# Kernel optimization log

Measured on AMD Instinct MI355X. Metric: run time of the kernel, lower is better.

The kernel has to match this reference:

```python
import jax, jax.numpy as jnp
import numpy as np

# Graph geometry: G complete graphs (molecules) of n nodes each.
N_PER_G, G, DEG = 64, 256, 16
H, D = 8, 8
IN_DIM = H * D      # 64
EDGE_DIM = 64
N = N_PER_G * G                      # 16384 nodes
EF = G * N_PER_G * N_PER_G           # 1,048,576 full edges
ES = G * N_PER_G * DEG               # 262,144 sparse edges
SCALE = float(np.sqrt(D))


def _edges():
    n = N_PER_G
    # full graph: all (i -> j) pairs per block, edge id = b*n*n + i*n + j
    ij = np.arange(n * n)
    i, j = ij // n, ij % n
    b = np.arange(G)[:, None]
    src_full = (b * n + i[None, :]).reshape(-1).astype(np.int32)
    dst_full = (b * n + j[None, :]).reshape(-1).astype(np.int32)
    # sparse graph: each dst j receives from DEG distinct sources (j+1..j+DEG mod n)
    jj = np.arange(n)[:, None]
    kk = np.arange(DEG)[None, :]
    ii = (jj + 1 + kk) % n
    eid_block = (ii * n + jj).reshape(-1)                 # [n*DEG]
    sparse_eid = (np.arange(G)[:, None] * n * n + eid_block[None, :]).reshape(-1).astype(np.int32)
    return jnp.asarray(src_full), jnp.asarray(dst_full), jnp.asarray(sparse_eid)


def setup_inputs() -> dict:
    key = jax.random.key(0)
    ks = jax.random.split(key, 16)
    w = lambda k, shape, s=0.05: s * jax.random.normal(k, shape, jnp.float32)
    src_full, dst_full, sparse_eid = _edges()
    return dict(
        h=jax.random.normal(ks[0], (N, IN_DIM), jnp.float32),
        e=jax.random.normal(ks[1], (ES, EDGE_DIM), jnp.float32),
        adj2=jax.random.uniform(ks[2], (EF,), jnp.float32),
        rel_pos_3d=jax.random.normal(ks[3], (EF, H), jnp.float32),
        Wq=w(ks[4], (H * D, IN_DIM)), bq=jnp.zeros((H * D,), jnp.float32),
        Wk=w(ks[5], (H * D, IN_DIM)), bk=jnp.zeros((H * D,), jnp.float32),
        Wv=w(ks[6], (H * D, IN_DIM)), bv=jnp.zeros((H * D,), jnp.float32),
        Wpe=w(ks[7], (H, EDGE_DIM)), bpe=jnp.zeros((H,), jnp.float32),
        Wap=w(ks[8], (EDGE_DIM, H)), bap=jnp.zeros((EDGE_DIM,), jnp.float32),
        Wo=w(ks[9], (H * D, H * D)), bo=jnp.zeros((H * D,), jnp.float32),
        Woe=w(ks[10], (EDGE_DIM, EDGE_DIM)), boe=jnp.zeros((EDGE_DIM,), jnp.float32),
        src_full=src_full, dst_full=dst_full, sparse_eid=sparse_eid,
    )


def reference(h, e, adj2, rel_pos_3d, Wq, bq, Wk, bk, Wv, bv, Wpe, bpe,
              Wap, bap, Wo, bo, Woe, boe, src_full, dst_full, sparse_eid):
    Qh = (h @ Wq.T + bq).reshape(N, H, D)
    Kh = (h @ Wk.T + bk).reshape(N, H, D)
    Vh = (h @ Wv.T + bv).reshape(N, H, D)
    proj_e = e @ Wpe.T + bpe                                   # [ES, H]
    # edge-wise QK dot (src=K, dst=Q), scaled, then gaussian-decay + rel-pos bias
    score = jnp.sum(Kh[src_full] * Qh[dst_full], axis=-1) / SCALE   # [EF, H]
    score = score * adj2[:, None] + rel_pos_3d                      # [EF, H]
    # gather sparse-subgraph scores, project for edge output, add proj_e bias
    sc_sp = score[sparse_eid]                                        # [ES, H]
    e_out_raw = sc_sp @ Wap.T + bap                                  # [ES, EDGE_DIM]
    score = score.at[sparse_eid].set(sc_sp + proj_e)
    # edge softmax over incoming edges of each destination node
    logits = jnp.clip(score, -5.0, 5.0)
    m = jax.ops.segment_max(logits, dst_full, num_segments=N)
    ex = jnp.exp(logits - m[dst_full])
    den = jax.ops.segment_sum(ex, dst_full, num_segments=N)
    attn = ex / den[dst_full]                                        # [EF, H]
    # weighted scatter-sum of source values
    wV = jax.ops.segment_sum(Vh[src_full] * attn[..., None], dst_full, num_segments=N)
    h_out = wV.reshape(N, H * D) @ Wo.T + bo
    e_out = (e_out_raw + e) @ Woe.T + boe
    return h_out, e_out
```

## Files before the change

kernel.cpp:

```cpp
#include <hip/hip_runtime.h>


__global__ __launch_bounds__(512, 2) void qkvpe_kernel(
    const float* __restrict__ h,
    const float* __restrict__ e,
    const float* __restrict__ Wq, const float* __restrict__ bq,
    const float* __restrict__ Wk, const float* __restrict__ bk,
    const float* __restrict__ Wv, const float* __restrict__ bv,
    const float* __restrict__ Wpe, const float* __restrict__ bpe,
    float* __restrict__ Qs, float* __restrict__ Ks, float* __restrict__ Vs,
    float* __restrict__ PEs)
{
    const int t = threadIdx.x;
    if (blockIdx.x < 256) {
        const int b    = blockIdx.x;
        const int lane = t & 63;
        const int wu   = __builtin_amdgcn_readfirstlane(t >> 6);
        const float* hrow = h + (size_t)(b * 64 + lane) * 64;
        float accQ[8], accK[8], accV[8];
        #pragma unroll
        for (int cc = 0; cc < 8; ++cc) {
            const int c = wu * 8 + cc;
            accQ[cc] = bq[c]; accK[cc] = bk[c]; accV[cc] = bv[c];
        }
        #pragma unroll 1
        for (int k0 = 0; k0 < 4; ++k0) {
            float hv[16];
            #pragma unroll
            for (int u = 0; u < 4; ++u) {
                const float4 x = ((const float4*)hrow)[k0 * 4 + u];
                hv[u*4+0] = x.x; hv[u*4+1] = x.y; hv[u*4+2] = x.z; hv[u*4+3] = x.w;
            }
            #pragma unroll
            for (int cc = 0; cc < 8; ++cc) {
                const int c = wu * 8 + cc;
                const float* wq  = Wq + c * 64 + k0 * 16;
                const float* wk  = Wk + c * 64 + k0 * 16;
                const float* wvp = Wv + c * 64 + k0 * 16;
                #pragma unroll
                for (int k = 0; k < 16; ++k) {
                    accQ[cc] = fmaf(hv[k], wq[k],  accQ[cc]);
                    accK[cc] = fmaf(hv[k], wk[k],  accK[cc]);
                    accV[cc] = fmaf(hv[k], wvp[k], accV[cc]);
                }
            }
        }
        const size_t o = (size_t)(b * 64 + lane) * 64 + wu * 8;
        *(float4*)(Qs + o)     = make_float4(accQ[0], accQ[1], accQ[2], accQ[3]);
        *(float4*)(Qs + o + 4) = make_float4(accQ[4], accQ[5], accQ[6], accQ[7]);
        *(float4*)(Ks + o)     = make_float4(accK[0], accK[1], accK[2], accK[3]);
        *(float4*)(Ks + o + 4) = make_float4(accK[4], accK[5], accK[6], accK[7]);
        *(float4*)(Vs + o)     = make_float4(accV[0], accV[1], accV[2], accV[3]);
        *(float4*)(Vs + o + 4) = make_float4(accV[4], accV[5], accV[6], accV[7]);
    } else {
        const int row = (blockIdx.x - 256) * 512 + t;
        const float* erow = e + (size_t)row * 64;
        float acc[8];
        #pragma unroll
        for (int h2 = 0; h2 < 8; ++h2) acc[h2] = bpe[h2];
        #pragma unroll 1
        for (int k0 = 0; k0 < 4; ++k0) {
            float ev[16];
            #pragma unroll
            for (int u = 0; u < 4; ++u) {
                const float4 x = ((const float4*)erow)[k0 * 4 + u];
                ev[u*4+0] = x.x; ev[u*4+1] = x.y; ev[u*4+2] = x.z; ev[u*4+3] = x.w;
            }
            #pragma unroll
            for (int h2 = 0; h2 < 8; ++h2) {
                const float* wp = Wpe + h2 * 64 + k0 * 16;
                #pragma unroll
                for (int k = 0; k < 16; ++k)
                    acc[h2] = fmaf(ev[k], wp[k], acc[h2]);
            }
        }
        float* p0 = PEs + (size_t)row * 8;
        *(float4*)(p0)     = make_float4(acc[0], acc[1], acc[2], acc[3]);
        *(float4*)(p0 + 4) = make_float4(acc[4], acc[5], acc[6], acc[7]);
    }
}

__global__ __launch_bounds__(1024, 2) void attn_kernel(
    const float* __restrict__ Qs, const float* __restrict__ Ks,
    const float* __restrict__ Vs, const float* __restrict__ PEs,
    const float* __restrict__ adj2,
    const float* __restrict__ rel,
    const float* __restrict__ Wo, const float* __restrict__ bo,
    float* __restrict__ h_out,
    float* __restrict__ scsp)
{
    __shared__ float shK[64 * 64];
    __shared__ float shV[64 * 64];
    __shared__ float shPE[512 * 8];
    __shared__ float shRed[256 * 9];

    const int b2   = blockIdx.x;
    const int b    = b2 >> 1;
    const int joff = (b2 & 1) << 5;
    const int t    = threadIdx.x;

    const int j_local = (t >> 3) & 31;
    const int hh      = t & 7;
    const int q4      = t >> 8;
    const int j       = joff + j_local;

    {
        const int r  = t >> 4;
        const int gh = t & 15;
        const int g  = gh >> 1, lo = (gh & 1) * 4;
        const int d  = r * 64 + ((g ^ (r & 7)) << 3) + lo;
        const int so = r * 64 + g * 8 + lo;
        shK[d + 0] = Ks[(size_t)b * 4096 + so + 0];
        shK[d + 1] = Ks[(size_t)b * 4096 + so + 1];
        shK[d + 2] = Ks[(size_t)b * 4096 + so + 2];
        shK[d + 3] = Ks[(size_t)b * 4096 + so + 3];
        shV[d + 0] = Vs[(size_t)b * 4096 + so + 0];
        shV[d + 1] = Vs[(size_t)b * 4096 + so + 1];
        shV[d + 2] = Vs[(size_t)b * 4096 + so + 2];
        shV[d + 3] = Vs[(size_t)b * 4096 + so + 3];
        *(float4*)&shPE[t * 4] =
            *(const float4*)(PEs + ((size_t)b * 1024 + joff * 16) * 8 + t * 4);
    }
    float q[8];
    {
        const float* qp = Qs + (size_t)(b * 64 + j) * 64 + hh * 8;
        const float4 a = *(const float4*)qp;
        const float4 c = *(const float4*)(qp + 4);
        q[0]=a.x; q[1]=a.y; q[2]=a.z; q[3]=a.w;
        q[4]=c.x; q[5]=c.y; q[6]=c.z; q[7]=c.w;
    }
    __syncthreads();

    float den = 0.f;
    float wv[8] = {0.f,0.f,0.f,0.f,0.f,0.f,0.f,0.f};
    const float* relP = rel  + (size_t)b * 32768 + (size_t)(joff + j_local) * 8 + hh;
    const float* adjP = adj2 + (size_t)b * 4096 + j;
    const float inv_scale = 0.35355339059327379f;
    #pragma unroll 4
    for (int it = 0; it < 16; ++it) {
        const int i  = (q4 << 4) + it;
        const float rp = relP[(size_t)i * 512];
        const float a2 = adjP[(size_t)i * 64];
        const int kb = i * 64 + ((hh ^ (i & 7)) << 3);
        const float4 kA = *(const float4*)&shK[kb];
        const float4 kB = *(const float4*)&shK[kb + 4];
        float s;
        s = kA.x * q[0];
        s = fmaf(kA.y, q[1], s); s = fmaf(kA.z, q[2], s); s = fmaf(kA.w, q[3], s);
        s = fmaf(kB.x, q[4], s); s = fmaf(kB.y, q[5], s); s = fmaf(kB.z, q[6], s);
        s = fmaf(kB.w, q[7], s);
        s = fmaf(s * inv_scale, a2, rp);
        const int kidx = (i - j - 1) & 63;
        if (kidx < 16) {
            const int x = (j_local * 16 + kidx) * 8 + hh;
            const float pe = shPE[x];
            shPE[x] = s;
            s += pe;
        }
        s = fminf(fmaxf(s, -5.f), 5.f);
        const float ex = __expf(s);
        den += ex;
        const float4 vA = *(const float4*)&shV[kb];
        const float4 vB = *(const float4*)&shV[kb + 4];
        wv[0] = fmaf(ex, vA.x, wv[0]); wv[1] = fmaf(ex, vA.y, wv[1]);
        wv[2] = fmaf(ex, vA.z, wv[2]); wv[3] = fmaf(ex, vA.w, wv[3]);
        wv[4] = fmaf(ex, vB.x, wv[4]); wv[5] = fmaf(ex, vB.y, wv[5]);
        wv[6] = fmaf(ex, vB.z, wv[6]); wv[7] = fmaf(ex, vB.w, wv[7]);
    }
    const int jh = t & 255;
    if (q4 == 0) {
        #pragma unroll
        for (int u = 0; u < 8; ++u) shRed[jh * 9 + u] = wv[u];
        shRed[jh * 9 + 8] = den;
    }
    __syncthreads();
    if (q4 == 1) {
        #pragma unroll
        for (int u = 0; u < 8; ++u) shRed[jh * 9 + u] += wv[u];
        shRed[jh * 9 + 8] += den;
    }
    __syncthreads();
    if (q4 == 2) {
        #pragma unroll
        for (int u = 0; u < 8; ++u) shRed[jh * 9 + u] += wv[u];
        shRed[jh * 9 + 8] += den;
    }
    __syncthreads();
    if (q4 == 3) {
        #pragma unroll
        for (int u = 0; u < 8; ++u) shRed[jh * 9 + u] += wv[u];
        shRed[jh * 9 + 8] += den;
    }
    __syncthreads();

    {
        const int row = t >> 1, pp = t & 1;
        *(float4*)(scsp + (size_t)((size_t)b * 1024 + joff * 16 + row) * 8 + pp * 4) =
            *(const float4*)&shPE[row * 8 + pp * 4];
    }
    if (t < 256) {
        const float* rd = &shRed[t * 9];
        const float id = 1.f / rd[8];
        float* wp = &shK[(t >> 3) * 64 + (t & 7) * 8];
        *(float4*)(wp)     = make_float4(rd[0]*id, rd[1]*id, rd[2]*id, rd[3]*id);
        *(float4*)(wp + 4) = make_float4(rd[4]*id, rd[5]*id, rd[6]*id, rd[7]*id);
    }
    __syncthreads();

    {
        const int rl = t >> 5;
        const int c0 = (t & 31) * 2;
        float acc[2];
        acc[0] = bo[c0]; acc[1] = bo[c0 + 1];
        #pragma unroll 1
        for (int k0 = 0; k0 < 4; ++k0) {
            float tv[16];
            #pragma unroll
            for (int u = 0; u < 4; ++u) {
                const float4 x = *(const float4*)&shK[rl * 64 + k0 * 16 + u * 4];
                tv[u*4+0] = x.x; tv[u*4+1] = x.y; tv[u*4+2] = x.z; tv[u*4+3] = x.w;
            }
            #pragma unroll
            for (int u = 0; u < 2; ++u) {
                const float* wo = Wo + (c0 + u) * 64 + k0 * 16;
                #pragma unroll
                for (int k = 0; k < 16; ++k)
                    acc[u] = fmaf(tv[k], wo[k], acc[u]);
            }
        }
        float* orow = h_out + (size_t)(b * 64 + joff + rl) * 64 + c0;
        *(float2*)orow = make_float2(acc[0], acc[1]);
    }
}

__global__ void prep_kernel(const float* __restrict__ Wap, const float* __restrict__ bap,
                            const float* __restrict__ Woe, const float* __restrict__ boe,
                            float* __restrict__ M2, float* __restrict__ Tm, int hasT)
{
    const int tg = blockIdx.x * 64 + threadIdx.x;
    if (tg < 512) {
        const int c = tg >> 3, hq = tg & 7;
        float s = 0.f;
        #pragma unroll 8
        for (int k = 0; k < 64; ++k) s = fmaf(Woe[c * 64 + k], Wap[k * 8 + hq], s);
        M2[tg] = s;
    } else if (tg < 576) {
        const int c = tg - 512;
        float s = boe[c];
        #pragma unroll 8
        for (int k = 0; k < 64; ++k) s = fmaf(bap[k], Woe[c * 64 + k], s);
        M2[512 + c] = s;
    } else if (hasT && tg < 576 + 73 * 64) {
        const int idx = tg - 576;
        const int k = idx >> 6, c = idx & 63;
        float v;
        if (k < 64) {
            v = Woe[c * 64 + k];
        } else if (k < 72) {
            const int hq = k - 64;
            v = 0.f;
            #pragma unroll 8
            for (int kk = 0; kk < 64; ++kk)
                v = fmaf(Woe[c * 64 + kk], Wap[kk * 8 + hq], v);
        } else {
            v = boe[c];
            #pragma unroll 8
            for (int kk = 0; kk < 64; ++kk)
                v = fmaf(bap[kk], Woe[c * 64 + kk], v);
        }
        Tm[k * 64 + c] = v;
    }
}

__global__ __launch_bounds__(256, 2) void eoutT_kernel(
    const float* __restrict__ e,
    const float* __restrict__ scsp,
    const float* __restrict__ Tm,
    float* __restrict__ e_out)
{
    __shared__ float shET[72 * 69];
    __shared__ float shTm[73 * 64];

    const int t    = threadIdx.x;
    const int base = blockIdx.x * 64;

    {
        const int r0 = t >> 2, qq = t & 3;
        const float* ep = e + (size_t)(base + r0) * 64 + qq * 16;
        #pragma unroll
        for (int v = 0; v < 4; ++v) {
            const float4 x = ((const float4*)ep)[v];
            const int c = qq * 16 + v * 4;
            shET[(c + 0) * 69 + r0] = x.x;
            shET[(c + 1) * 69 + r0] = x.y;
            shET[(c + 2) * 69 + r0] = x.z;
            shET[(c + 3) * 69 + r0] = x.w;
        }
    }
    if (t < 128) {
        const int r = t >> 1, pp = t & 1;
        const float4 s4 = *(const float4*)(scsp + (size_t)(base + r) * 8 + pp * 4);
        shET[(64 + pp * 4 + 0) * 69 + r] = s4.x;
        shET[(64 + pp * 4 + 1) * 69 + r] = s4.y;
        shET[(64 + pp * 4 + 2) * 69 + r] = s4.z;
        shET[(64 + pp * 4 + 3) * 69 + r] = s4.w;
    }
    #pragma unroll
    for (int v = 0; v < 5; ++v) {
        const int fi = v * 256 + t;
        if (fi < 1168)
            *(float4*)&shTm[fi * 4] = *(const float4*)(Tm + fi * 4);
    }
    __syncthreads();

    const int rq = t >> 4;
    const int cq = t & 15;

    float acc[16];
    {
        const float4 bcv = *(const float4*)&shTm[72 * 64 + cq * 4];
        #pragma unroll
        for (int ri = 0; ri < 4; ++ri) {
            acc[ri*4+0] = bcv.x; acc[ri*4+1] = bcv.y;
            acc[ri*4+2] = bcv.z; acc[ri*4+3] = bcv.w;
        }
    }
    #pragma unroll
    for (int k = 0; k < 72; ++k) {
        const float4 ev = *(const float4*)&shET[k * 69 + rq * 4];
        const float4 wk = *(const float4*)&shTm[k * 64 + cq * 4];
        acc[0]  = fmaf(ev.x, wk.x, acc[0]);  acc[1]  = fmaf(ev.x, wk.y, acc[1]);
        acc[2]  = fmaf(ev.x, wk.z, acc[2]);  acc[3]  = fmaf(ev.x, wk.w, acc[3]);
        acc[4]  = fmaf(ev.y, wk.x, acc[4]);  acc[5]  = fmaf(ev.y, wk.y, acc[5]);
        acc[6]  = fmaf(ev.y, wk.z, acc[6]);  acc[7]  = fmaf(ev.y, wk.w, acc[7]);
        acc[8]  = fmaf(ev.z, wk.x, acc[8]);  acc[9]  = fmaf(ev.z, wk.y, acc[9]);
        acc[10] = fmaf(ev.z, wk.z, acc[10]); acc[11] = fmaf(ev.z, wk.w, acc[11]);
        acc[12] = fmaf(ev.w, wk.x, acc[12]); acc[13] = fmaf(ev.w, wk.y, acc[13]);
        acc[14] = fmaf(ev.w, wk.z, acc[14]); acc[15] = fmaf(ev.w, wk.w, acc[15]);
    }
    #pragma unroll
    for (int ri = 0; ri < 4; ++ri) {
        float* orow = e_out + (size_t)(base + rq * 4 + ri) * 64 + cq * 4;
        *(float4*)orow = make_float4(acc[ri*4+0], acc[ri*4+1], acc[ri*4+2], acc[ri*4+3]);
    }
}

__global__ __launch_bounds__(256, 2) void eout_kernel(
    const float* __restrict__ e,
    const float* __restrict__ scsp,
    const float* __restrict__ Woe,
    const float* __restrict__ M2g,
    float* __restrict__ e_out)
{
    __shared__ float shE[64 * 64];
    __shared__ float shS[64 * 8];
    const int t    = threadIdx.x;
    const int base = blockIdx.x * 64;
    {
        const int r = t >> 2, qq = t & 3;
        const float* ep = e + (size_t)(base + r) * 64 + qq * 16;
        #pragma unroll
        for (int u = 0; u < 4; ++u) {
            const float4 x = ((const float4*)ep)[u];
            const int cc = qq * 4 + u;
            *(float4*)&shE[r * 64 + ((cc ^ (r & 15)) << 2)] = x;
        }
    }
    if (t < 128) {
        const int r = t >> 1, pp = t & 1;
        *(float4*)&shS[r * 8 + pp * 4] =
            *(const float4*)(scsp + (size_t)(base + r) * 8 + pp * 4);
    }
    __syncthreads();
    const int w = __builtin_amdgcn_readfirstlane(t >> 6);
    const int r = t & 63;
    float sc[8];
    {
        const float4 a  = *(const float4*)&shS[r * 8];
        const float4 c4 = *(const float4*)&shS[r * 8 + 4];
        sc[0]=a.x; sc[1]=a.y; sc[2]=a.z; sc[3]=a.w;
        sc[4]=c4.x; sc[5]=c4.y; sc[6]=c4.z; sc[7]=c4.w;
    }
    float acc[16];
    #pragma unroll
    for (int u = 0; u < 16; ++u) {
        const int c = w * 16 + u;
        float s = M2g[512 + c];
        #pragma unroll
        for (int hq = 0; hq < 8; ++hq)
            s = fmaf(sc[hq], M2g[c * 8 + hq], s);
        acc[u] = s;
    }
    #pragma unroll
    for (int k0 = 0; k0 < 4; ++k0) {
        float ev[16];
        #pragma unroll
        for (int v = 0; v < 4; ++v) {
            const int cc = k0 * 4 + v;
            const float4 x = *(const float4*)&shE[r * 64 + ((cc ^ (r & 15)) << 2)];
            ev[v*4+0] = x.x; ev[v*4+1] = x.y; ev[v*4+2] = x.z; ev[v*4+3] = x.w;
        }
        #pragma unroll
        for (int u = 0; u < 16; ++u) {
            const float* wr = Woe + (w * 16 + u) * 64 + k0 * 16;
            #pragma unroll
            for (int k = 0; k < 16; ++k)
                acc[u] = fmaf(ev[k], wr[k], acc[u]);
        }
    }
    float* orow = e_out + (size_t)(base + r) * 64 + w * 16;
    #pragma unroll
    for (int u = 0; u < 4; ++u)
        *(float4*)&orow[u * 4] =
            make_float4(acc[u*4+0], acc[u*4+1], acc[u*4+2], acc[u*4+3]);
}

extern "C" void kernel_launch(void* const* d_in, const int* in_sizes, int n_in,
                              void* d_out, int out_size, void* d_ws, size_t ws_size,
                              hipStream_t stream) {
    const float* h    = (const float*)d_in[0];
    const float* e    = (const float*)d_in[1];
    const float* adj2 = (const float*)d_in[2];
    const float* rel  = (const float*)d_in[3];
    const float* Wq   = (const float*)d_in[4];  const float* bq  = (const float*)d_in[5];
    const float* Wk   = (const float*)d_in[6];  const float* bk  = (const float*)d_in[7];
    const float* Wv   = (const float*)d_in[8];  const float* bv  = (const float*)d_in[9];
    const float* Wpe  = (const float*)d_in[10]; const float* bpe = (const float*)d_in[11];
    const float* Wap  = (const float*)d_in[12]; const float* bap = (const float*)d_in[13];
    const float* Wo   = (const float*)d_in[14]; const float* bo  = (const float*)d_in[15];
    const float* Woe  = (const float*)d_in[16]; const float* boe = (const float*)d_in[17];

    float* out  = (float*)d_out;
    float* hout = out;
    float* eout = out + 16384 * 64;
    float* Qs   = eout;
    float* Ks   = eout + 1048576;
    float* Vs   = eout + 2097152;
    float* PEs  = eout + 3145728;
    float* ws   = (float*)d_ws;
    float* scsp = ws;
    float* M2g  = ws + 2097152;
    float* Tm   = ws + 2098176;
    const int hasT = (ws_size >= (size_t)(2098176 + 73 * 64) * sizeof(float)) ? 1 : 0;

    prep_kernel<<<dim3(82), dim3(64), 0, stream>>>(Wap, bap, Woe, boe, M2g, Tm, hasT);
    qkvpe_kernel<<<dim3(768), dim3(512), 0, stream>>>(
        h, e, Wq, bq, Wk, bk, Wv, bv, Wpe, bpe, Qs, Ks, Vs, PEs);
    attn_kernel<<<dim3(512), dim3(1024), 0, stream>>>(
        Qs, Ks, Vs, PEs, adj2, rel, Wo, bo, hout, scsp);
    if (hasT)
        eoutT_kernel<<<dim3(4096), dim3(256), 0, stream>>>(e, scsp, Tm, eout);
    else
        eout_kernel<<<dim3(4096), dim3(256), 0, stream>>>(e, scsp, Woe, M2g, eout);
}
```

Before: 130.9 us.

## Restructure attention so each thread loops all sources; split output projection into own kernel

The attention kernel now assigns one thread per (destination, head) pair and loops over all 64 sources. The loop starts at the 16 sparse neighbours so the edge-bias add and score capture happen in registers. This removes the LDS staging of K/V/PE, the four-way shared-memory reduction and its barriers. K and V are read straight from global/cache, and the normalized wV is written to the h_out buffer. A new hout_kernel then applies Wo in place with a register-tiled shared-memory GEMM. The trade-offs are a quarter as many threads, longer serial loops, and rel/adj accesses that now vary the source index per lane and so coalesce less well. It also adds an extra launch and a global round trip for wV.

```diff
diff --git a/kernel.cpp b/kernel.cpp
--- a/kernel.cpp
+++ b/kernel.cpp
@@ -80,47 +80,27 @@
     }
 }
 
-__global__ __launch_bounds__(1024, 2) void attn_kernel(
+__global__ __launch_bounds__(256, 2) void attn_kernel(
     const float* __restrict__ Qs, const float* __restrict__ Ks,
     const float* __restrict__ Vs, const float* __restrict__ PEs,
     const float* __restrict__ adj2,
     const float* __restrict__ rel,
-    const float* __restrict__ Wo, const float* __restrict__ bo,
-    float* __restrict__ h_out,
+    float* __restrict__ wVg,
     float* __restrict__ scsp)
 {
-    __shared__ float shK[64 * 64];
-    __shared__ float shV[64 * 64];
-    __shared__ float shPE[512 * 8];
-    __shared__ float shRed[256 * 9];
-
     const int b2   = blockIdx.x;
     const int b    = b2 >> 1;
     const int joff = (b2 & 1) << 5;
     const int t    = threadIdx.x;
-
-    const int j_local = (t >> 3) & 31;
-    const int hh      = t & 7;
-    const int q4      = t >> 8;
-    const int j       = joff + j_local;
-
-    {
-        const int r  = t >> 4;
-        const int gh = t & 15;
-        const int g  = gh >> 1, lo = (gh & 1) * 4;
-        const int d  = r * 64 + ((g ^ (r & 7)) << 3) + lo;
-        const int so = r * 64 + g * 8 + lo;
-        shK[d + 0] = Ks[(size_t)b * 4096 + so + 0];
-        shK[d + 1] = Ks[(size_t)b * 4096 + so + 1];
-        shK[d + 2] = Ks[(size_t)b * 4096 + so + 2];
-        shK[d + 3] = Ks[(size_t)b * 4096 + so + 3];
-        shV[d + 0] = Vs[(size_t)b * 4096 + so + 0];
-        shV[d + 1] = Vs[(size_t)b * 4096 + so + 1];
-        shV[d + 2] = Vs[(size_t)b * 4096 + so + 2];
-        shV[d + 3] = Vs[(size_t)b * 4096 + so + 3];
-        *(float4*)&shPE[t * 4] =
-            *(const float4*)(PEs + ((size_t)b * 1024 + joff * 16) * 8 + t * 4);
-    }
+    const int j    = joff + (t >> 3);
+    const int hh   = t & 7;
+
+    const float* kB   = Ks + (size_t)b * 4096 + hh * 8;
+    const float* vB   = Vs + (size_t)b * 4096 + hh * 8;
+    const float* relP = rel + ((size_t)b * 4096 + j) * 8 + hh;
+    const float* adjP = adj2 + (size_t)b * 4096 + j;
+    const float* peP  = PEs + ((size_t)b * 1024 + j * 16) * 8 + hh;
+
     float q[8];
     {
         const float* qp = Qs + (size_t)(b * 64 + j) * 64 + hh * 8;
@@ -129,107 +109,137 @@
         q[0]=a.x; q[1]=a.y; q[2]=a.z; q[3]=a.w;
         q[4]=c.x; q[5]=c.y; q[6]=c.z; q[7]=c.w;
     }
-    __syncthreads();
 
     float den = 0.f;
     float wv[8] = {0.f,0.f,0.f,0.f,0.f,0.f,0.f,0.f};
-    const float* relP = rel  + (size_t)b * 32768 + (size_t)(joff + j_local) * 8 + hh;
-    const float* adjP = adj2 + (size_t)b * 4096 + j;
+    float sc[16];
     const float inv_scale = 0.35355339059327379f;
-    #pragma unroll 4
-    for (int it = 0; it < 16; ++it) {
-        const int i  = (q4 << 4) + it;
+
+    #pragma unroll
+    for (int m = 0; m < 16; ++m) {
+        const int i = (j + 1 + m) & 63;
+        const float4 kA = *(const float4*)(kB + i * 64);
+        const float4 kBv = *(const float4*)(kB + i * 64 + 4);
         const float rp = relP[(size_t)i * 512];
         const float a2 = adjP[(size_t)i * 64];
-        const int kb = i * 64 + ((hh ^ (i & 7)) << 3);
-        const float4 kA = *(const float4*)&shK[kb];
-        const float4 kB = *(const float4*)&shK[kb + 4];
-        float s;
-        s = kA.x * q[0];
+        const float pe = peP[m * 8];
+        float s = kA.x * q[0];
         s = fmaf(kA.y, q[1], s); s = fmaf(kA.z, q[2], s); s = fmaf(kA.w, q[3], s);
-        s = fmaf(kB.x, q[4], s); s = fmaf(kB.y, q[5], s); s = fmaf(kB.z, q[6], s);
-        s = fmaf(kB.w, q[7], s);
+        s = fmaf(kBv.x, q[4], s); s = fmaf(kBv.y, q[5], s); s = fmaf(kBv.z, q[6], s);
+        s = fmaf(kBv.w, q[7], s);
         s = fmaf(s * inv_scale, a2, rp);
-        const int kidx = (i - j - 1) & 63;
-        if (kidx < 16) {
-            const int x = (j_local * 16 + kidx) * 8 + hh;
-            const float pe = shPE[x];
-            shPE[x] = s;
-            s += pe;
-        }
+        sc[m] = s;
+        s += pe;
         s = fminf(fmaxf(s, -5.f), 5.f);
         const float ex = __expf(s);
         den += ex;
-        const float4 vA = *(const float4*)&shV[kb];
-        const float4 vB = *(const float4*)&shV[kb + 4];
+        const float4 vA = *(const float4*)(vB + i * 64);
+        const float4 vBv = *(const float4*)(vB + i * 64 + 4);
         wv[0] = fmaf(ex, vA.x, wv[0]); wv[1] = fmaf(ex, vA.y, wv[1]);
         wv[2] = fmaf(ex, vA.z, wv[2]); wv[3] = fmaf(ex, vA.w, wv[3]);
-        wv[4] = fmaf(ex, vB.x, wv[4]); wv[5] = fmaf(ex, vB.y, wv[5]);
-        wv[6] = fmaf(ex, vB.z, wv[6]); wv[7] = fmaf(ex, vB.w, wv[7]);
-    }
-    const int jh = t & 255;
-    if (q4 == 0) {
-        #pragma unroll
-        for (int u = 0; u < 8; ++u) shRed[jh * 9 + u] = wv[u];
-        shRed[jh * 9 + 8] = den;
+        wv[4] = fmaf(ex, vBv.x, wv[4]); wv[5] = fmaf(ex, vBv.y, wv[5]);
+        wv[6] = fmaf(ex, vBv.z, wv[6]); wv[7] = fmaf(ex, vBv.w, wv[7]);
+    }
+    #pragma unroll 8
+    for (int m = 16; m < 64; ++m) {
+        const int i = (j + 1 + m) & 63;
+        const float4 kA = *(const float4*)(kB + i * 64);
+        const float4 kBv = *(const float4*)(kB + i * 64 + 4);
+        const float rp = relP[(size_t)i * 512];
+        const float a2 = adjP[(size_t)i * 64];
+        float s = kA.x * q[0];
+        s = fmaf(kA.y, q[1], s); s = fmaf(kA.z, q[2], s); s = fmaf(kA.w, q[3], s);
+        s = fmaf(kBv.x, q[4], s); s = fmaf(kBv.y, q[5], s); s = fmaf(kBv.z, q[6], s);
+        s = fmaf(kBv.w, q[7], s);
+        s = fmaf(s * inv_scale, a2, rp);
+        s = fminf(fmaxf(s, -5.f), 5.f);
+        const float ex = __expf(s);
+        den += ex;
+        const float4 vA = *(const float4*)(vB + i * 64);
+        const float4 vBv = *(const float4*)(vB + i * 64 + 4);
+        wv[0] = fmaf(ex, vA.x, wv[0]); wv[1] = fmaf(ex, vA.y, wv[1]);
+        wv[2] = fmaf(ex, vA.z, wv[2]); wv[3] = fmaf(ex, vA.w, wv[3]);
+        wv[4] = fmaf(ex, vBv.x, wv[4]); wv[5] = fmaf(ex, vBv.y, wv[5]);
+        wv[6] = fmaf(ex, vBv.z, wv[6]); wv[7] = fmaf(ex, vBv.w, wv[7]);
+    }
+
+    float* sp = scsp + ((size_t)b * 1024 + j * 16) * 8 + hh;
+    #pragma unroll
+    for (int m = 0; m < 16; ++m) sp[m * 8] = sc[m];
+
+    const float id = 1.f / den;
+    float* wp = wVg + (size_t)(b * 64 + j) * 64 + hh * 8;
+    *(float4*)(wp)     = make_float4(wv[0]*id, wv[1]*id, wv[2]*id, wv[3]*id);
+    *(float4*)(wp + 4) = make_float4(wv[4]*id, wv[5]*id, wv[6]*id, wv[7]*id);
+}
+
+__global__ __launch_bounds__(256, 2) void hout_kernel(
+    const float* __restrict__ wVg,
+    const float* __restrict__ Wo, const float* __restrict__ bo,
+    float* __restrict__ h_out)
+{
+    __shared__ float shWT[64 * 69];
+    __shared__ float shWoT[64 * 65];
+
+    const int t    = threadIdx.x;
+    const int base = blockIdx.x * 64;
+
+    {
+        const int r0 = t >> 2, qq = t & 3;
+        const float* ep = wVg + (size_t)(base + r0) * 64 + qq * 16;
+        #pragma unroll
+        for (int v = 0; v < 4; ++v) {
+            const float4 x = ((const float4*)ep)[v];
+            const int c = qq * 16 + v * 4;
+            shWT[(c + 0) * 69 + r0] = x.x;
+            shWT[(c + 1) * 69 + r0] = x.y;
+            shWT[(c + 2) * 69 + r0] = x.z;
+            shWT[(c + 3) * 69 + r0] = x.w;
+        }
+    }
+    {
+        const int c0 = t >> 2, qq = t & 3;
+        const float* wp = Wo + c0 * 64 + qq * 16;
+        #pragma unroll
+        for (int v = 0; v < 4; ++v) {
+            const float4 x = ((const float4*)wp)[v];
+            const int k = qq * 16 + v * 4;
+            shWoT[(k + 0) * 65 + c0] = x.x;
+            shWoT[(k + 1) * 65 + c0] = x.y;
+            shWoT[(k + 2) * 65 + c0] = x.z;
+            shWoT[(k + 3) * 65 + c0] = x.w;
+        }
     }
     __syncthreads();
-    if (q4 == 1) {
-        #pragma unroll
-        for (int u = 0; u < 8; ++u) shRed[jh * 9 + u] += wv[u];
-        shRed[jh * 9 + 8] += den;
-    }
-    __syncthreads();
-    if (q4 == 2) {
-        #pragma unroll
-        for (int u = 0; u < 8; ++u) shRed[jh * 9 + u] += wv[u];
-        shRed[jh * 9 + 8] += den;
-    }
-    __syncthreads();
-    if (q4 == 3) {
-        #pragma unroll
-        for (int u = 0; u < 8; ++u) shRed[jh * 9 + u] += wv[u];
-        shRed[jh * 9 + 8] += den;
-    }
-    __syncthreads();
-
-    {
-        const int row = t >> 1, pp = t & 1;
-        *(float4*)(scsp + (size_t)((size_t)b * 1024 + joff * 16 + row) * 8 + pp * 4) =
-            *(const float4*)&shPE[row * 8 + pp * 4];
-    }
-    if (t < 256) {
-        const float* rd = &shRed[t * 9];
-        const float id = 1.f / rd[8];
-        float* wp = &shK[(t >> 3) * 64 + (t & 7) * 8];
-        *(float4*)(wp)     = make_float4(rd[0]*id, rd[1]*id, rd[2]*id, rd[3]*id);
-        *(float4*)(wp + 4) = make_float4(rd[4]*id, rd[5]*id, rd[6]*id, rd[7]*id);
-    }
-    __syncthreads();
-
-    {
-        const int rl = t >> 5;
-        const int c0 = (t & 31) * 2;
-        float acc[2];
-        acc[0] = bo[c0]; acc[1] = bo[c0 + 1];
-        #pragma unroll 1
-        for (int k0 = 0; k0 < 4; ++k0) {
-            float tv[16];
-            #pragma unroll
-            for (int u = 0; u < 4; ++u) {
-                const float4 x = *(const float4*)&shK[rl * 64 + k0 * 16 + u * 4];
-                tv[u*4+0] = x.x; tv[u*4+1] = x.y; tv[u*4+2] = x.z; tv[u*4+3] = x.w;
-            }
-            #pragma unroll
-            for (int u = 0; u < 2; ++u) {
-                const float* wo = Wo + (c0 + u) * 64 + k0 * 16;
-                #pragma unroll
-                for (int k = 0; k < 16; ++k)
-                    acc[u] = fmaf(tv[k], wo[k], acc[u]);
-            }
-        }
-        float* orow = h_out + (size_t)(b * 64 + joff + rl) * 64 + c0;
-        *(float2*)orow = make_float2(acc[0], acc[1]);
+
+    const int rq = t >> 4;
+    const int cq = t & 15;
+    float acc[16];
+    {
+        const float4 bv = *(const float4*)(bo + cq * 4);
+        #pragma unroll
+        for (int ri = 0; ri < 4; ++ri) {
+            acc[ri*4+0] = bv.x; acc[ri*4+1] = bv.y;
+            acc[ri*4+2] = bv.z; acc[ri*4+3] = bv.w;
+        }
+    }
+    #pragma unroll
+    for (int k = 0; k < 64; ++k) {
+        const float4 ev = *(const float4*)&shWT[k * 69 + rq * 4];
+        const float4 wk = *(const float4*)&shWoT[k * 65 + cq * 4];
+        acc[0]  = fmaf(ev.x, wk.x, acc[0]);  acc[1]  = fmaf(ev.x, wk.y, acc[1]);
+        acc[2]  = fmaf(ev.x, wk.z, acc[2]);  acc[3]  = fmaf(ev.x, wk.w, acc[3]);
+        acc[4]  = fmaf(ev.y, wk.x, acc[4]);  acc[5]  = fmaf(ev.y, wk.y, acc[5]);
+        acc[6]  = fmaf(ev.y, wk.z, acc[6]);  acc[7]  = fmaf(ev.y, wk.w, acc[7]);
+        acc[8]  = fmaf(ev.z, wk.x, acc[8]);  acc[9]  = fmaf(ev.z, wk.y, acc[9]);
+        acc[10] = fmaf(ev.z, wk.z, acc[10]); acc[11] = fmaf(ev.z, wk.w, acc[11]);
+        acc[12] = fmaf(ev.w, wk.x, acc[12]); acc[13] = fmaf(ev.w, wk.y, acc[13]);
+        acc[14] = fmaf(ev.w, wk.z, acc[14]); acc[15] = fmaf(ev.w, wk.w, acc[15]);
+    }
+    #pragma unroll
+    for (int ri = 0; ri < 4; ++ri) {
+        float* orow = h_out + (size_t)(base + rq * 4 + ri) * 64 + cq * 4;
+        *(float4*)orow = make_float4(acc[ri*4+0], acc[ri*4+1], acc[ri*4+2], acc[ri*4+3]);
     }
 }
 
@@ -315,7 +325,6 @@
 
     const int rq = t >> 4;
     const int cq = t & 15;
-
     float acc[16];
     {
         const float4 bcv = *(const float4*)&shTm[72 * 64 + cq * 4];
@@ -446,8 +455,9 @@
     prep_kernel<<<dim3(82), dim3(64), 0, stream>>>(Wap, bap, Woe, boe, M2g, Tm, hasT);
     qkvpe_kernel<<<dim3(768), dim3(512), 0, stream>>>(
         h, e, Wq, bq, Wk, bk, Wv, bv, Wpe, bpe, Qs, Ks, Vs, PEs);
-    attn_kernel<<<dim3(512), dim3(1024), 0, stream>>>(
-        Qs, Ks, Vs, PEs, adj2, rel, Wo, bo, hout, scsp);
+    attn_kernel<<<dim3(512), dim3(256), 0, stream>>>(
+        Qs, Ks, Vs, PEs, adj2, rel, hout , scsp);
+    hout_kernel<<<dim3(256), dim3(256), 0, stream>>>(hout, Wo, bo, hout);
     if (hasT)
         eoutT_kernel<<<dim3(4096), dim3(256), 0, stream>>>(e, scsp, Tm, eout);
     else
```

Measured after the change: 130.8 us. About the same (-0.1%).

## Stage rel/adj tiles in LDS for attention; register-resident edge-output GEMM

Applied to the files above, without the earlier changes.

The attention kernel now loads each block's rel_pos_3d and adj2 tiles into shared memory with coalesced float4 loads before the score loop. Previously each thread did strided scalar global reads inside the loop. This adds about 77KB of LDS, so launch bounds drop to one block per CU. Separately, eoutT_kernel no longer uses a shared-memory transposed tile: each thread holds one full edge row in 72 registers and reads a 16-column slice of Tm through wave-uniform scalar loads. The cost is higher register pressure.

```diff
diff --git a/kernel.cpp b/kernel.cpp
--- a/kernel.cpp
+++ b/kernel.cpp
@@ -80,7 +80,7 @@
     }
 }
 
-__global__ __launch_bounds__(1024, 2) void attn_kernel(
+__global__ __launch_bounds__(1024, 1) void attn_kernel(
     const float* __restrict__ Qs, const float* __restrict__ Ks,
     const float* __restrict__ Vs, const float* __restrict__ PEs,
     const float* __restrict__ adj2,
@@ -93,6 +93,8 @@
     __shared__ float shV[64 * 64];
     __shared__ float shPE[512 * 8];
     __shared__ float shRed[256 * 9];
+    __shared__ float shRel[64 * 264];
+    __shared__ float shAdj[64 * 36];
 
     const int b2   = blockIdx.x;
     const int b    = b2 >> 1;
@@ -104,6 +106,22 @@
     const int q4      = t >> 8;
     const int j       = joff + j_local;
 
+    {
+        const float* rbase = rel + (size_t)b * 32768 + joff * 8;
+        #pragma unroll
+        for (int u = 0; u < 4; ++u) {
+            const int fidx = u * 1024 + t;
+            const int i    = fidx >> 6;
+            const int c4   = fidx & 63;
+            *(float4*)&shRel[i * 264 + c4 * 4] =
+                *(const float4*)(rbase + (size_t)i * 512 + c4 * 4);
+        }
+    }
+    if (t < 512) {
+        const int i2 = t >> 3, grp = t & 7;
+        *(float4*)&shAdj[i2 * 36 + grp * 4] =
+            *(const float4*)(adj2 + (size_t)b * 4096 + i2 * 64 + joff + grp * 4);
+    }
     {
         const int r  = t >> 4;
         const int gh = t & 15;
@@ -133,14 +151,13 @@
 
     float den = 0.f;
     float wv[8] = {0.f,0.f,0.f,0.f,0.f,0.f,0.f,0.f};
-    const float* relP = rel  + (size_t)b * 32768 + (size_t)(joff + j_local) * 8 + hh;
-    const float* adjP = adj2 + (size_t)b * 4096 + j;
+    const int jh = t & 255;
     const float inv_scale = 0.35355339059327379f;
     #pragma unroll 4
     for (int it = 0; it < 16; ++it) {
         const int i  = (q4 << 4) + it;
-        const float rp = relP[(size_t)i * 512];
-        const float a2 = adjP[(size_t)i * 64];
+        const float rp = shRel[i * 264 + jh];
+        const float a2 = shAdj[i * 36 + j_local];
         const int kb = i * 64 + ((hh ^ (i & 7)) << 3);
         const float4 kA = *(const float4*)&shK[kb];
         const float4 kB = *(const float4*)&shK[kb + 4];
@@ -167,7 +184,6 @@
         wv[4] = fmaf(ex, vB.x, wv[4]); wv[5] = fmaf(ex, vB.y, wv[5]);
         wv[6] = fmaf(ex, vB.z, wv[6]); wv[7] = fmaf(ex, vB.w, wv[7]);
     }
-    const int jh = t & 255;
     if (q4 == 0) {
         #pragma unroll
         for (int u = 0; u < 8; ++u) shRed[jh * 9 + u] = wv[u];
@@ -278,71 +294,40 @@
     const float* __restrict__ Tm,
     float* __restrict__ e_out)
 {
-    __shared__ float shET[72 * 69];
-    __shared__ float shTm[73 * 64];
-
-    const int t    = threadIdx.x;
-    const int base = blockIdx.x * 64;
-
-    {
-        const int r0 = t >> 2, qq = t & 3;
-        const float* ep = e + (size_t)(base + r0) * 64 + qq * 16;
-        #pragma unroll
-        for (int v = 0; v < 4; ++v) {
+    const int t   = threadIdx.x;
+    const int r   = t & 63;
+    const int w   = __builtin_amdgcn_readfirstlane(t >> 6);
+    const int row = blockIdx.x * 64 + r;
+
+    float ev[72];
+    {
+        const float* ep = e + (size_t)row * 64;
+        #pragma unroll
+        for (int v = 0; v < 16; ++v) {
             const float4 x = ((const float4*)ep)[v];
-            const int c = qq * 16 + v * 4;
-            shET[(c + 0) * 69 + r0] = x.x;
-            shET[(c + 1) * 69 + r0] = x.y;
-            shET[(c + 2) * 69 + r0] = x.z;
-            shET[(c + 3) * 69 + r0] = x.w;
-        }
-    }
-    if (t < 128) {
-        const int r = t >> 1, pp = t & 1;
-        const float4 s4 = *(const float4*)(scsp + (size_t)(base + r) * 8 + pp * 4);
-        shET[(64 + pp * 4 + 0) * 69 + r] = s4.x;
-        shET[(64 + pp * 4 + 1) * 69 + r] = s4.y;
-        shET[(64 + pp * 4 + 2) * 69 + r] = s4.z;
-        shET[(64 + pp * 4 + 3) * 69 + r] = s4.w;
-    }
-    #pragma unroll
-    for (int v = 0; v < 5; ++v) {
-        const int fi = v * 256 + t;
-        if (fi < 1168)
-            *(float4*)&shTm[fi * 4] = *(const float4*)(Tm + fi * 4);
-    }
-    __syncthreads();
-
-    const int rq = t >> 4;
-    const int cq = t & 15;
-
+            ev[v*4+0] = x.x; ev[v*4+1] = x.y; ev[v*4+2] = x.z; ev[v*4+3] = x.w;
+        }
+        const float4 s0 = *(const float4*)(scsp + (size_t)row * 8);
+        const float4 s1 = *(const float4*)(scsp + (size_t)row * 8 + 4);
+        ev[64]=s0.x; ev[65]=s0.y; ev[66]=s0.z; ev[67]=s0.w;
+        ev[68]=s1.x; ev[69]=s1.y; ev[70]=s1.z; ev[71]=s1.w;
+    }
+    const float* wbase = Tm + w * 16;
     float acc[16];
-    {
-        const float4 bcv = *(const float4*)&shTm[72 * 64 + cq * 4];
-        #pragma unroll
-        for (int ri = 0; ri < 4; ++ri) {
-            acc[ri*4+0] = bcv.x; acc[ri*4+1] = bcv.y;
-            acc[ri*4+2] = bcv.z; acc[ri*4+3] = bcv.w;
-        }
-    }
+    #pragma unroll
+    for (int u = 0; u < 16; ++u) acc[u] = wbase[72 * 64 + u];
     #pragma unroll
     for (int k = 0; k < 72; ++k) {
-        const float4 ev = *(const float4*)&shET[k * 69 + rq * 4];
-        const float4 wk = *(const float4*)&shTm[k * 64 + cq * 4];
-        acc[0]  = fmaf(ev.x, wk.x, acc[0]);  acc[1]  = fmaf(ev.x, wk.y, acc[1]);
-        acc[2]  = fmaf(ev.x, wk.z, acc[2]);  acc[3]  = fmaf(ev.x, wk.w, acc[3]);
-        acc[4]  = fmaf(ev.y, wk.x, acc[4]);  acc[5]  = fmaf(ev.y, wk.y, acc[5]);
-        acc[6]  = fmaf(ev.y, wk.z, acc[6]);  acc[7]  = fmaf(ev.y, wk.w, acc[7]);
-        acc[8]  = fmaf(ev.z, wk.x, acc[8]);  acc[9]  = fmaf(ev.z, wk.y, acc[9]);
-        acc[10] = fmaf(ev.z, wk.z, acc[10]); acc[11] = fmaf(ev.z, wk.w, acc[11]);
-        acc[12] = fmaf(ev.w, wk.x, acc[12]); acc[13] = fmaf(ev.w, wk.y, acc[13]);
-        acc[14] = fmaf(ev.w, wk.z, acc[14]); acc[15] = fmaf(ev.w, wk.w, acc[15]);
-    }
-    #pragma unroll
-    for (int ri = 0; ri < 4; ++ri) {
-        float* orow = e_out + (size_t)(base + rq * 4 + ri) * 64 + cq * 4;
-        *(float4*)orow = make_float4(acc[ri*4+0], acc[ri*4+1], acc[ri*4+2], acc[ri*4+3]);
-    }
+        const float* wk = wbase + k * 64;
+        #pragma unroll
+        for (int u = 0; u < 16; ++u)
+            acc[u] = fmaf(ev[k], wk[u], acc[u]);
+    }
+    float* orow = e_out + (size_t)row * 64 + w * 16;
+    #pragma unroll
+    for (int u = 0; u < 4; ++u)
+        *(float4*)&orow[u * 4] =
+            make_float4(acc[u*4+0], acc[u*4+1], acc[u*4+2], acc[u*4+3]);
 }
 
 __global__ __launch_bounds__(256, 2) void eout_kernel(
```

Result: slower. 141.4 us (+8.0%).
